# Performance work log

Hardware: AMD Instinct MI355X
Metric: run time of the kernel (lower is better)

Reference implementation:

```python
import jax, jax.numpy as jnp
import numpy as np

EMB = 1024
HEADS = 16
HEAD_SZ = 64
INNER = 4 * EMB
EPS = 1e-5


def layer_norm(x, g, b):
    mu = jnp.mean(x, axis=-1, keepdims=True)
    var = jnp.mean(jnp.square(x - mu), axis=-1, keepdims=True)
    return (x - mu) * jax.lax.rsqrt(var + EPS) * g + b


def setup_inputs() -> dict:
    key = jax.random.key(0)
    ks = jax.random.split(key, 12)
    s = 1.0 / np.sqrt(EMB)
    si = 1.0 / np.sqrt(INNER)
    return {
        "x": jax.random.normal(ks[0], (4, 2048, EMB), dtype=jnp.float32),
        "Wq": jax.random.uniform(ks[1], (EMB, HEADS * HEAD_SZ), jnp.float32, -s, s),
        "Wk": jax.random.uniform(ks[2], (EMB, HEADS * HEAD_SZ), jnp.float32, -s, s),
        "Wv": jax.random.uniform(ks[3], (EMB, HEADS * HEAD_SZ), jnp.float32, -s, s),
        "Wo": jax.random.uniform(ks[4], (HEADS * HEAD_SZ, EMB), jnp.float32, -s, s),
        "bo": jax.random.uniform(ks[5], (EMB,), jnp.float32, -s, s),
        "g1": jnp.ones((EMB,), jnp.float32),
        "b1": jnp.zeros((EMB,), jnp.float32),
        "W1": jax.random.uniform(ks[6], (EMB, INNER), jnp.float32, -s, s),
        "bf1": jax.random.uniform(ks[7], (INNER,), jnp.float32, -s, s),
        "W2": jax.random.uniform(ks[8], (INNER, EMB), jnp.float32, -si, si),
        "bf2": jax.random.uniform(ks[9], (EMB,), jnp.float32, -si, si),
        "g2": jnp.ones((EMB,), jnp.float32),
        "b2": jnp.zeros((EMB,), jnp.float32),
    }


def reference(x, Wq, Wk, Wv, Wo, bo, g1, b1, W1, bf1, W2, bf2, g2, b2):
    bs, seq, _ = x.shape
    # QKV projections -> [b, h, s, d]
    def split_heads(t):
        return t.reshape(bs, seq, HEADS, HEAD_SZ).transpose(0, 2, 1, 3)
    q = split_heads(x @ Wq)
    k = split_heads(x @ Wk)
    v = split_heads(x @ Wv)
    # scaled dot-product attention (vanilla, no mask; pdrop=0)
    attn = jnp.einsum("bhqd,bhkd->bhqk", q, k) / np.sqrt(HEAD_SZ)
    attn = jax.nn.softmax(attn, axis=-1)
    out = jnp.einsum("bhqk,bhkd->bhqd", attn, v)
    out = out.transpose(0, 2, 1, 3).reshape(bs, seq, HEADS * HEAD_SZ)
    out = out @ Wo + bo
    # residual + post-LN
    h = layer_norm(x + out, g1, b1)
    # FFN
    ff = jax.nn.relu(h @ W1 + bf1) @ W2 + bf2
    return layer_norm(h + ff, g2, b2)
```

## Files before the change

kernel.cpp:

```cpp
#include <hip/hip_runtime.h>
#include <stdint.h>

#define DEVI __device__ __forceinline__

typedef __attribute__((ext_vector_type(8))) short bf16x8;
typedef __attribute__((ext_vector_type(4))) float f32x4;
typedef unsigned short u16;
typedef uint32_t u32;

constexpr int EMB = 1024, SEQ = 2048, NTOK = 8192;
constexpr int HEADS = 16, HD = 64, INNER = 4096;

DEVI u16 f2b(float f) {
  u32 u = __float_as_uint(f);
  return (u16)((u + 0x7FFFu + ((u >> 16) & 1u)) >> 16);
}

DEVI u32 pk2(float lo, float hi) {
  u32 r;
  asm("v_cvt_pk_bf16_f32 %0, %1, %2" : "=v"(r) : "v"(lo), "v"(hi));
  return r;
}

DEVI float exp2v(float x) {
  float r;
  asm("v_exp_f32 %0, %1" : "=v"(r) : "v"(x));
  return r;
}

DEVI void gload16(const void* g, void* l) {
  __builtin_amdgcn_global_load_lds(
      (const __attribute__((address_space(1))) void*)g,
      (__attribute__((address_space(3))) void*)l, 16, 0, 0);
}

DEVI int xcd_swz(int bid, int nwg) { return (bid & 7) * (nwg >> 3) + (bid >> 3); }

DEVI int vperm(int k) {
  int g = (k >> 2) & 3, j = k & 3, s2 = k >> 4;
  return ((s2 >> 1) << 5) + (g << 3) + ((s2 & 1) << 2) + j;
}

__global__ __launch_bounds__(256) void k_cvt(const float* __restrict__ src,
                                             u16* __restrict__ dst, int n4) {
  int i = blockIdx.x * 256 + threadIdx.x;
  if (i >= n4) return;
  float4 v = ((const float4*)src)[i];
  ushort4 o = {f2b(v.x), f2b(v.y), f2b(v.z), f2b(v.w)};
  ((ushort4*)dst)[i] = o;
}

__global__ __launch_bounds__(256) void k_cvtT(const float* __restrict__ src,
                                              u16* __restrict__ dst, int K, int N) {
  __shared__ float t[32][33];
  int bk = blockIdx.x % (K >> 5), bn = blockIdx.x / (K >> 5);
  int tx = threadIdx.x & 31, ty = threadIdx.x >> 5;
#pragma unroll
  for (int i = 0; i < 4; i++)
    t[ty + i * 8][tx] = src[(size_t)(bk * 32 + ty + i * 8) * N + bn * 32 + tx];
  __syncthreads();
#pragma unroll
  for (int i = 0; i < 4; i++)
    dst[(size_t)(bn * 32 + ty + i * 8) * K + bk * 32 + tx] = f2b(t[tx][ty + i * 8]);
}

template <int EPI>
__global__ __launch_bounds__(512, 2) void k_gemm8(
    const u16* __restrict__ A, const u16* __restrict__ BT, int M, int N, int K,
    u16* __restrict__ ob0, u16* __restrict__ ob1, u16* __restrict__ ob2,
    float* __restrict__ of0, const float* __restrict__ bias,
    const float* __restrict__ res) {
  __shared__ u16 LDS[3][24576];
  const int tid = threadIdx.x;
  const int lane = tid & 63, w = tid >> 6;
  const int wr = w >> 1, wc = w & 1;
  const int g = lane >> 4, c = lane & 15;
  const int nbx = N >> 7;
  const int bid = xcd_swz(blockIdx.x, gridDim.x);
  const int by = bid / nbx, bx = bid % nbx;
  const int row0 = by << 8, col0 = bx << 7;
  const int NK = K >> 6;

  const f32x4 z4 = {0.f, 0.f, 0.f, 0.f};
  f32x4 acc[4][4];
#pragma unroll
  for (int m = 0; m < 4; m++)
#pragma unroll
    for (int n = 0; n < 4; n++) acc[m][n] = z4;

  auto stageA = [&](int t) {
    const int k0 = t << 6;
    char* base = (char*)&LDS[t % 3][0];
#pragma unroll
    for (int i = 0; i < 4; i++) {
      int s = tid + (i << 9);
      int r = s >> 3, cb = s & 7;
      gload16(A + (size_t)(row0 + r) * K + (k0 + ((cb ^ (r & 7)) << 3)),
              base + s * 16);
    }
  };
  auto stageB = [&](int t) {
    const int k0 = t << 6;
    char* base = (char*)&LDS[t % 3][0] + 32768;
#pragma unroll
    for (int i = 0; i < 2; i++) {
      int s = tid + (i << 9);
      int r = s >> 3, cb = s & 7;
      gload16(BT + (size_t)(col0 + r) * K + (k0 + ((cb ^ (r & 7)) << 3)),
              base + s * 16);
    }
  };

  stageA(0); stageB(0);
  stageA(1); stageB(1);
  asm volatile("s_waitcnt vmcnt(6)" ::: "memory");
  __builtin_amdgcn_s_barrier();

  for (int t = 0; t < NK; t++) {
    const char* Ab = (const char*)&LDS[t % 3][0];
    const char* Bb = Ab + 32768;

    bf16x8 af[4][2], bfr[2][2];
#pragma unroll
    for (int m = 0; m < 4; m++)
#pragma unroll
      for (int kk = 0; kk < 2; kk++) {
        int r = wr * 64 + m * 16 + c;
        af[m][kk] = *(const bf16x8*)(Ab + ((r * 128 + kk * 64 + g * 16) ^ ((r & 7) << 4)));
      }
#pragma unroll
    for (int ni = 0; ni < 2; ni++)
#pragma unroll
      for (int kk = 0; kk < 2; kk++) {
        int rb = wc * 64 + ni * 16 + c;
        bfr[ni][kk] = *(const bf16x8*)(Bb + ((rb * 128 + kk * 64 + g * 16) ^ ((rb & 7) << 4)));
      }
    if (t + 2 < NK) stageA(t + 2);
    __builtin_amdgcn_sched_barrier(0);
    __builtin_amdgcn_s_barrier();
    asm volatile("s_waitcnt lgkmcnt(0)" ::: "memory");
    __builtin_amdgcn_sched_barrier(0);
    __builtin_amdgcn_s_setprio(1);
#pragma unroll
    for (int m = 0; m < 4; m++)
#pragma unroll
      for (int ni = 0; ni < 2; ni++)
#pragma unroll
        for (int kk = 0; kk < 2; kk++)
          acc[m][ni] = __builtin_amdgcn_mfma_f32_16x16x32_bf16(af[m][kk], bfr[ni][kk],
                                                               acc[m][ni], 0, 0, 0);
    __builtin_amdgcn_s_setprio(0);
    __builtin_amdgcn_sched_barrier(0);
    __builtin_amdgcn_s_barrier();

#pragma unroll
    for (int ni = 0; ni < 2; ni++)
#pragma unroll
      for (int kk = 0; kk < 2; kk++) {
        int rb = wc * 64 + 32 + ni * 16 + c;
        bfr[ni][kk] = *(const bf16x8*)(Bb + ((rb * 128 + kk * 64 + g * 16) ^ ((rb & 7) << 4)));
      }
    if (t + 2 < NK) stageB(t + 2);
    __builtin_amdgcn_sched_barrier(0);
    __builtin_amdgcn_s_barrier();
    asm volatile("s_waitcnt lgkmcnt(0)" ::: "memory");
    __builtin_amdgcn_sched_barrier(0);
    __builtin_amdgcn_s_setprio(1);
#pragma unroll
    for (int m = 0; m < 4; m++)
#pragma unroll
      for (int ni = 0; ni < 2; ni++)
#pragma unroll
        for (int kk = 0; kk < 2; kk++)
          acc[m][2 + ni] = __builtin_amdgcn_mfma_f32_16x16x32_bf16(af[m][kk], bfr[ni][kk],
                                                                   acc[m][2 + ni], 0, 0, 0);
    __builtin_amdgcn_s_setprio(0);
    __builtin_amdgcn_sched_barrier(0);
    if (t + 2 < NK)
      asm volatile("s_waitcnt vmcnt(6)" ::: "memory");
    else if (t + 1 < NK)
      asm volatile("s_waitcnt vmcnt(0)" ::: "memory");
    __builtin_amdgcn_s_barrier();
  }

#pragma unroll
  for (int m = 0; m < 4; m++) {
#pragma unroll
    for (int n = 0; n < 4; n++) {
      int ocol = col0 + wc * 64 + n * 16 + c;
      int orow_base = row0 + wr * 64 + m * 16 + 4 * g;
      if constexpr (EPI == 0) {
        int which = ocol >> 10, rem = ocol & 1023;
        int h = rem >> 6, d = rem & 63;
        if (which == 2) {
          int b = orow_base >> 11, sl = orow_base & 2047;
          int blk = sl & ~63, k4 = sl & 63;
          int p = vperm(k4);
          int bh = b * HEADS + h;
          ushort4 vv = {f2b(acc[m][n][0]), f2b(acc[m][n][1]),
                        f2b(acc[m][n][2]), f2b(acc[m][n][3])};
          *(ushort4*)(ob2 + ((size_t)bh * HD + d) * SEQ + blk + p) = vv;
        } else {
#pragma unroll
          for (int r = 0; r < 4; r++) {
            int orow = orow_base + r;
            int b = orow >> 11, s = orow & 2047;
            int bh = b * HEADS + h;
            float av = acc[m][n][r];
            if (which == 0)
              ob0[((size_t)bh * SEQ + s) * HD + d] = f2b(av * 0.1803368801111244f);
            else
              ob1[((size_t)bh * SEQ + s) * HD + d] = f2b(av);
          }
        }
      } else if constexpr (EPI == 1) {
        float bia = bias[ocol];
#pragma unroll
        for (int r = 0; r < 4; r++) {
          int orow = orow_base + r;
          of0[(size_t)orow * N + ocol] =
              acc[m][n][r] + bia + res[(size_t)orow * N + ocol];
        }
      } else if constexpr (EPI == 2) {
        float bia = bias[ocol];
#pragma unroll
        for (int r = 0; r < 4; r++) {
          int orow = orow_base + r;
          float v = acc[m][n][r] + bia;
          ob0[(size_t)orow * N + ocol] = f2b(v > 0.f ? v : 0.f);
        }
      } else {
        float bia = bias[ocol];
#pragma unroll
        for (int r = 0; r < 4; r++) {
          int orow = orow_base + r;
          of0[(size_t)orow * N + ocol] = acc[m][n][r] + bia;
        }
      }
    }
  }
}

__global__ __launch_bounds__(256, 4) void k_attn(const u16* __restrict__ q,
                                                 const u16* __restrict__ kb,
                                                 const u16* __restrict__ vT,
                                                 u16* __restrict__ attn) {
  __shared__ u16 Ks[2][64 * 64];
  __shared__ u16 Vs[2][64 * 64];
  const int tid = threadIdx.x, lane = tid & 63, w = tid >> 6;
  const int g = lane >> 4, c = lane & 15;
  const int blk = xcd_swz(blockIdx.x, gridDim.x);
  const int bh = blk >> 5, qb = blk & 31;
  const int b = bh >> 4, h = bh & 15;
  const u16* qh = q + (size_t)bh * SEQ * HD;
  const u16* kh = kb + (size_t)bh * SEQ * HD;
  const u16* vh = vT + (size_t)bh * HD * SEQ;
  const int qr = qb * 64 + w * 16 + c;
  bf16x8 qf0 = *(const bf16x8*)(qh + (size_t)qr * HD + 8 * g);
  bf16x8 qf1 = *(const bf16x8*)(qh + (size_t)qr * HD + 32 + 8 * g);

  const f32x4 z4 = {0.f, 0.f, 0.f, 0.f};
  f32x4 O[4];
#pragma unroll
  for (int m = 0; m < 4; m++) O[m] = z4;
  float mI = -3.0e38f, lI = 0.f;

  auto stage = [&](int kt, int buf) {
    const int kv0 = kt * 64;
#pragma unroll
    for (int i = 0; i < 2; i++) {
      int s = tid + (i << 8);
      int r = s >> 3, cb = s & 7;
      gload16(kh + (size_t)(kv0 + r) * HD + ((cb ^ (r & 7)) << 3),
              (char*)Ks[buf] + s * 16);
    }
#pragma unroll
    for (int i = 0; i < 2; i++) {
      int s = tid + (i << 8);
      int r = s >> 3, cb = s & 7;
      gload16(vh + (size_t)r * SEQ + kv0 + ((cb ^ (r & 7)) << 3),
              (char*)Vs[buf] + s * 16);
    }
  };

  stage(0, 0);
  __syncthreads();
  int cur = 0;
  constexpr int NT = SEQ / 64;
  for (int kt = 0; kt < NT; kt++) {
    if (kt + 1 < NT) stage(kt + 1, cur ^ 1);

    const char* ksb = (const char*)Ks[cur];
    f32x4 sc[4];
    __builtin_amdgcn_s_setprio(1);
#pragma unroll
    for (int m = 0; m < 4; m++) {
      int r = 16 * m + c;
      int sw = (r & 7) << 4;
      bf16x8 kf0 = *(const bf16x8*)(ksb + ((r * 128 + g * 16) ^ sw));
      bf16x8 kf1 = *(const bf16x8*)(ksb + ((r * 128 + 64 + g * 16) ^ sw));
      f32x4 a = z4;
      a = __builtin_amdgcn_mfma_f32_16x16x32_bf16(kf0, qf0, a, 0, 0, 0);
      a = __builtin_amdgcn_mfma_f32_16x16x32_bf16(kf1, qf1, a, 0, 0, 0);
      sc[m] = a;
    }
    __builtin_amdgcn_s_setprio(0);

    float mx = sc[0][0];
#pragma unroll
    for (int m = 0; m < 4; m++)
#pragma unroll
      for (int r = 0; r < 4; r++) mx = fmaxf(mx, sc[m][r]);
    mx = fmaxf(mx, __shfl_xor(mx, 16));
    mx = fmaxf(mx, __shfl_xor(mx, 32));
    if (!__all(mx - mI <= 8.f)) {
      float mNew = fmaxf(mI, mx);
      float alpha = exp2v(mI - mNew);
      lI *= alpha;
#pragma unroll
      for (int m = 0; m < 4; m++)
#pragma unroll
        for (int r = 0; r < 4; r++) O[m][r] *= alpha;
      mI = mNew;
    }
    float p[4][4];
    float rs = 0.f;
#pragma unroll
    for (int m = 0; m < 4; m++)
#pragma unroll
      for (int r = 0; r < 4; r++) {
        p[m][r] = exp2v(sc[m][r] - mI);
        rs += p[m][r];
      }
    rs += __shfl_xor(rs, 16);
    rs += __shfl_xor(rs, 32);
    lI += rs;

    union V8w { bf16x8 v; u32 w4[4]; };
    V8w pa0, pa1;
    pa0.w4[0] = pk2(p[0][0], p[0][1]); pa0.w4[1] = pk2(p[0][2], p[0][3]);
    pa0.w4[2] = pk2(p[1][0], p[1][1]); pa0.w4[3] = pk2(p[1][2], p[1][3]);
    pa1.w4[0] = pk2(p[2][0], p[2][1]); pa1.w4[1] = pk2(p[2][2], p[2][3]);
    pa1.w4[2] = pk2(p[3][0], p[3][1]); pa1.w4[3] = pk2(p[3][2], p[3][3]);

    const char* vsb = (const char*)Vs[cur];
    __builtin_amdgcn_s_setprio(1);
#pragma unroll
    for (int m = 0; m < 4; m++) {
      int d = 16 * m + c;
      int sw = (d & 7) << 4;
      bf16x8 v0 = *(const bf16x8*)(vsb + ((d * 128 + g * 16) ^ sw));
      bf16x8 v1 = *(const bf16x8*)(vsb + ((d * 128 + 64 + g * 16) ^ sw));
      O[m] = __builtin_amdgcn_mfma_f32_16x16x32_bf16(v0, pa0.v, O[m], 0, 0, 0);
      O[m] = __builtin_amdgcn_mfma_f32_16x16x32_bf16(v1, pa1.v, O[m], 0, 0, 0);
    }
    __builtin_amdgcn_s_setprio(0);

    __syncthreads();
    cur ^= 1;
  }

  float inv = 1.f / lI;
#pragma unroll
  for (int m = 0; m < 4; m++) {
    ushort4 ov = {f2b(O[m][0] * inv), f2b(O[m][1] * inv),
                  f2b(O[m][2] * inv), f2b(O[m][3] * inv)};
    int col = h * 64 + 16 * m + 4 * g;
    *(ushort4*)(attn + ((size_t)(b * SEQ + qr)) * EMB + col) = ov;
  }
}

__global__ __launch_bounds__(256) void k_ln1(const float* __restrict__ y,
                                             const float* __restrict__ gw,
                                             const float* __restrict__ bw,
                                             float* __restrict__ hf,
                                             u16* __restrict__ hb) {
  const int row = blockIdx.x, tid = threadIdx.x, lane = tid & 63, w = tid >> 6;
  const float4 v = ((const float4*)(y + (size_t)row * EMB))[tid];
  float s = v.x + v.y + v.z + v.w;
  float s2 = v.x * v.x + v.y * v.y + v.z * v.z + v.w * v.w;
#pragma unroll
  for (int m = 1; m < 64; m <<= 1) {
    s += __shfl_xor(s, m);
    s2 += __shfl_xor(s2, m);
  }
  __shared__ float rs_[4], rq_[4];
  if (lane == 0) { rs_[w] = s; rq_[w] = s2; }
  __syncthreads();
  s = rs_[0] + rs_[1] + rs_[2] + rs_[3];
  s2 = rq_[0] + rq_[1] + rq_[2] + rq_[3];
  const float mu = s * (1.f / EMB);
  const float var = s2 * (1.f / EMB) - mu * mu;
  const float rstd = rsqrtf(var + 1e-5f);
  const float4 gg = ((const float4*)gw)[tid];
  const float4 bb = ((const float4*)bw)[tid];
  float4 o;
  o.x = (v.x - mu) * rstd * gg.x + bb.x;
  o.y = (v.y - mu) * rstd * gg.y + bb.y;
  o.z = (v.z - mu) * rstd * gg.z + bb.z;
  o.w = (v.w - mu) * rstd * gg.w + bb.w;
  ((float4*)(hf + (size_t)row * EMB))[tid] = o;
  ushort4 ob = {f2b(o.x), f2b(o.y), f2b(o.z), f2b(o.w)};
  ((ushort4*)(hb + (size_t)row * EMB))[tid] = ob;
}

__global__ __launch_bounds__(256) void k_ln2(const float* __restrict__ hf,
                                             const float* __restrict__ z,
                                             const float* __restrict__ gw,
                                             const float* __restrict__ bw,
                                             float* __restrict__ outp) {
  const int row = blockIdx.x, tid = threadIdx.x, lane = tid & 63, w = tid >> 6;
  float4 v = ((const float4*)(hf + (size_t)row * EMB))[tid];
  const float4 zz = ((const float4*)(z + (size_t)row * EMB))[tid];
  v.x += zz.x; v.y += zz.y; v.z += zz.z; v.w += zz.w;
  float s = v.x + v.y + v.z + v.w;
  float s2 = v.x * v.x + v.y * v.y + v.z * v.z + v.w * v.w;
#pragma unroll
  for (int m = 1; m < 64; m <<= 1) {
    s += __shfl_xor(s, m);
    s2 += __shfl_xor(s2, m);
  }
  __shared__ float rs_[4], rq_[4];
  if (lane == 0) { rs_[w] = s; rq_[w] = s2; }
  __syncthreads();
  s = rs_[0] + rs_[1] + rs_[2] + rs_[3];
  s2 = rq_[0] + rq_[1] + rq_[2] + rq_[3];
  const float mu = s * (1.f / EMB);
  const float var = s2 * (1.f / EMB) - mu * mu;
  const float rstd = rsqrtf(var + 1e-5f);
  const float4 gg = ((const float4*)gw)[tid];
  const float4 bb = ((const float4*)bw)[tid];
  float4 o;
  o.x = (v.x - mu) * rstd * gg.x + bb.x;
  o.y = (v.y - mu) * rstd * gg.y + bb.y;
  o.z = (v.z - mu) * rstd * gg.z + bb.z;
  o.w = (v.w - mu) * rstd * gg.w + bb.w;
  ((float4*)(outp + (size_t)row * EMB))[tid] = o;
}

extern "C" void kernel_launch(void* const* d_in, const int* in_sizes, int n_in,
                              void* d_out, int out_size, void* d_ws, size_t ws_size,
                              hipStream_t stream) {
  const float* x = (const float*)d_in[0];
  const float* Wq = (const float*)d_in[1];
  const float* Wk = (const float*)d_in[2];
  const float* Wv = (const float*)d_in[3];
  const float* Wo = (const float*)d_in[4];
  const float* bo = (const float*)d_in[5];
  const float* g1 = (const float*)d_in[6];
  const float* b1 = (const float*)d_in[7];
  const float* W1 = (const float*)d_in[8];
  const float* bf1 = (const float*)d_in[9];
  const float* W2 = (const float*)d_in[10];
  const float* bf2 = (const float*)d_in[11];
  const float* g2 = (const float*)d_in[12];
  const float* b2 = (const float*)d_in[13];
  float* out = (float*)d_out;

  char* ws = (char*)d_ws;
  size_t off = 0;
  auto alloc = [&](size_t bytes) {
    char* p = ws + off;
    off += (bytes + 255) & ~(size_t)255;
    return p;
  };
  u16* xb = (u16*)alloc((size_t)NTOK * EMB * 2);
  u16* wqkvT = (u16*)alloc((size_t)3072 * 1024 * 2);
  u16* qB = (u16*)alloc((size_t)NTOK * EMB * 2);
  u16* kB = (u16*)alloc((size_t)NTOK * EMB * 2);
  u16* vTB = (u16*)alloc((size_t)NTOK * EMB * 2);
  u16* woT = (u16*)alloc((size_t)1024 * 1024 * 2);
  u16* w1T = (u16*)alloc((size_t)4096 * 1024 * 2);
  u16* w2T = (u16*)alloc((size_t)1024 * 4096 * 2);
  float* y = (float*)alloc((size_t)NTOK * EMB * 4);
  u16* ff1 = (u16*)alloc((size_t)NTOK * INNER * 2);
  u16* attn = xb;
  float* hf = (float*)qB;
  u16* hb = vTB;
  float* z = y;

  k_cvt<<<NTOK * EMB / 4 / 256, 256, 0, stream>>>(x, xb, NTOK * EMB / 4);
  k_cvtT<<<1024, 256, 0, stream>>>(Wq, wqkvT, 1024, 1024);
  k_cvtT<<<1024, 256, 0, stream>>>(Wk, wqkvT + 1048576, 1024, 1024);
  k_cvtT<<<1024, 256, 0, stream>>>(Wv, wqkvT + 2097152, 1024, 1024);
  k_cvtT<<<1024, 256, 0, stream>>>(Wo, woT, 1024, 1024);
  k_cvtT<<<4096, 256, 0, stream>>>(W1, w1T, 1024, 4096);
  k_cvtT<<<4096, 256, 0, stream>>>(W2, w2T, 4096, 1024);
  k_gemm8<0><<<(NTOK / 256) * (3072 / 128), 512, 0, stream>>>(
      xb, wqkvT, NTOK, 3072, 1024, qB, kB, vTB, nullptr, nullptr, nullptr);
  k_attn<<<64 * 32, 256, 0, stream>>>(qB, kB, vTB, attn);
  k_gemm8<1><<<(NTOK / 256) * (1024 / 128), 512, 0, stream>>>(
      attn, woT, NTOK, 1024, 1024, nullptr, nullptr, nullptr, y, bo, x);
  k_ln1<<<NTOK, 256, 0, stream>>>(y, g1, b1, hf, hb);
  k_gemm8<2><<<(NTOK / 256) * (4096 / 128), 512, 0, stream>>>(
      hb, w1T, NTOK, 4096, 1024, ff1, nullptr, nullptr, nullptr, bf1, nullptr);
  k_gemm8<3><<<(NTOK / 256) * (1024 / 128), 512, 0, stream>>>(
      ff1, w2T, NTOK, 1024, 4096, nullptr, nullptr, nullptr, z, bf2, nullptr);
  k_ln2<<<NTOK, 256, 0, stream>>>(hf, z, g2, b2, out);
}
```

Before: 538.6 us.

## Add 256x256-tile GEMM kernel for QKV and FFN1 projections

```diff
diff --git a/kernel.cpp b/kernel.cpp
--- a/kernel.cpp
+++ b/kernel.cpp
@@ -62,6 +62,217 @@
 #pragma unroll
   for (int i = 0; i < 4; i++)
     dst[(size_t)(bn * 32 + ty + i * 8) * K + bk * 32 + tx] = f2b(t[tx][ty + i * 8]);
+}
+
+template <int EPI>
+__global__ __launch_bounds__(512, 2) void k_g256(
+    const u16* __restrict__ A, const u16* __restrict__ BT, int M, int N, int K,
+    u16* __restrict__ ob0, u16* __restrict__ ob1, u16* __restrict__ ob2,
+    float* __restrict__ of0, const float* __restrict__ bias,
+    const float* __restrict__ res) {
+  __shared__ u16 LDS[81920];
+  const int tid = threadIdx.x;
+  const int lane = tid & 63, w = tid >> 6;
+  const int wr = w >> 2, wc = w & 3;
+  const int g = lane >> 4, c = lane & 15;
+  const int nbx = N >> 8;
+  const int bid = xcd_swz(blockIdx.x, gridDim.x);
+  const int by = bid / nbx, bx = bid % nbx;
+  const int row0 = by << 8, col0 = bx << 8;
+  const int NK = K >> 6;
+
+  const f32x4 z4 = {0.f, 0.f, 0.f, 0.f};
+  f32x4 acc[8][4];
+#pragma unroll
+  for (int m = 0; m < 8; m++)
+#pragma unroll
+    for (int n = 0; n < 4; n++) acc[m][n] = z4;
+
+  auto stA = [&](int t, int h) {
+    const int k0 = t << 6;
+    char* base = (char*)LDS + (t % 3) * 32768 + h * 16384;
+#pragma unroll
+    for (int i = 0; i < 2; i++) {
+      int s = tid + (i << 9);
+      int r = (h << 7) + (s >> 3), cb = s & 7;
+      gload16(A + (size_t)(row0 + r) * K + (k0 + ((cb ^ (r & 7)) << 3)),
+              base + s * 16);
+    }
+  };
+  auto stB = [&](int t, int h) {
+    const int k0 = t << 6;
+    char* base = (char*)LDS + 98304 + (t & 1) * 32768 + h * 16384;
+#pragma unroll
+    for (int i = 0; i < 2; i++) {
+      int s = tid + (i << 9);
+      int r = (h << 7) + (s >> 3), cb = s & 7;
+      gload16(BT + (size_t)(col0 + r) * K + (k0 + ((cb ^ (r & 7)) << 3)),
+              base + s * 16);
+    }
+  };
+  auto rdA = [&](const char* Ab, int row, int kk) {
+    return *(const bf16x8*)(Ab + ((row * 128 + kk * 64 + g * 16) ^ ((row & 7) << 4)));
+  };
+
+  stA(0, 0); stA(0, 1);
+  stB(0, 0); stB(0, 1);
+  stA(1, 0); stA(1, 1);
+  asm volatile("s_waitcnt vmcnt(4)" ::: "memory");
+  __builtin_amdgcn_s_barrier();
+  __builtin_amdgcn_sched_barrier(0);
+
+  for (int t = 0; t < NK; t++) {
+    const char* Ab = (const char*)LDS + (t % 3) * 32768;
+    const char* Bb = (const char*)LDS + 98304 + (t & 1) * 32768;
+    bf16x8 af[4][2], b0[2][2], b1[2][2];
+
+#pragma unroll
+    for (int m = 0; m < 4; m++)
+#pragma unroll
+      for (int kk = 0; kk < 2; kk++) af[m][kk] = rdA(Ab, wr * 128 + m * 16 + c, kk);
+#pragma unroll
+    for (int n = 0; n < 2; n++)
+#pragma unroll
+      for (int kk = 0; kk < 2; kk++) b0[n][kk] = rdA(Bb, wc * 64 + n * 16 + c, kk);
+    if (t + 1 < NK) stB(t + 1, 0);
+    asm volatile("s_waitcnt lgkmcnt(8)" ::: "memory");
+    __builtin_amdgcn_sched_barrier(0);
+    __builtin_amdgcn_s_barrier();
+    asm volatile("s_waitcnt lgkmcnt(0)" ::: "memory");
+    __builtin_amdgcn_sched_barrier(0);
+    __builtin_amdgcn_s_setprio(1);
+#pragma unroll
+    for (int m = 0; m < 4; m++)
+#pragma unroll
+      for (int n = 0; n < 2; n++)
+#pragma unroll
+        for (int kk = 0; kk < 2; kk++)
+          acc[m][n] = __builtin_amdgcn_mfma_f32_16x16x32_bf16(af[m][kk], b0[n][kk],
+                                                              acc[m][n], 0, 0, 0);
+    __builtin_amdgcn_s_setprio(0);
+    __builtin_amdgcn_sched_barrier(0);
+    __builtin_amdgcn_s_barrier();
+
+#pragma unroll
+    for (int n = 0; n < 2; n++)
+#pragma unroll
+      for (int kk = 0; kk < 2; kk++)
+        b1[n][kk] = rdA(Bb, wc * 64 + 32 + n * 16 + c, kk);
+    if (t + 1 < NK) stB(t + 1, 1);
+    __builtin_amdgcn_sched_barrier(0);
+    __builtin_amdgcn_s_barrier();
+    asm volatile("s_waitcnt lgkmcnt(0)" ::: "memory");
+    __builtin_amdgcn_sched_barrier(0);
+    __builtin_amdgcn_s_setprio(1);
+#pragma unroll
+    for (int m = 0; m < 4; m++)
+#pragma unroll
+      for (int n = 0; n < 2; n++)
+#pragma unroll
+        for (int kk = 0; kk < 2; kk++)
+          acc[m][2 + n] = __builtin_amdgcn_mfma_f32_16x16x32_bf16(af[m][kk], b1[n][kk],
+                                                                  acc[m][2 + n], 0, 0, 0);
+    __builtin_amdgcn_s_setprio(0);
+    __builtin_amdgcn_sched_barrier(0);
+    __builtin_amdgcn_s_barrier();
+
+#pragma unroll
+    for (int m = 0; m < 4; m++)
+#pragma unroll
+      for (int kk = 0; kk < 2; kk++)
+        af[m][kk] = rdA(Ab, wr * 128 + 64 + m * 16 + c, kk);
+    if (t + 2 < NK) stA(t + 2, 0);
+    __builtin_amdgcn_sched_barrier(0);
+    __builtin_amdgcn_s_barrier();
+    asm volatile("s_waitcnt lgkmcnt(0)" ::: "memory");
+    __builtin_amdgcn_sched_barrier(0);
+    __builtin_amdgcn_s_setprio(1);
+#pragma unroll
+    for (int m = 0; m < 4; m++)
+#pragma unroll
+      for (int n = 0; n < 2; n++)
+#pragma unroll
+        for (int kk = 0; kk < 2; kk++)
+          acc[4 + m][n] = __builtin_amdgcn_mfma_f32_16x16x32_bf16(af[m][kk], b0[n][kk],
+                                                                  acc[4 + m][n], 0, 0, 0);
+    __builtin_amdgcn_s_setprio(0);
+    __builtin_amdgcn_sched_barrier(0);
+    __builtin_amdgcn_s_barrier();
+
+    if (t + 2 < NK) stA(t + 2, 1);
+    __builtin_amdgcn_sched_barrier(0);
+    __builtin_amdgcn_s_barrier();
+    __builtin_amdgcn_s_setprio(1);
+#pragma unroll
+    for (int m = 0; m < 4; m++)
+#pragma unroll
+      for (int n = 0; n < 2; n++)
+#pragma unroll
+        for (int kk = 0; kk < 2; kk++)
+          acc[4 + m][2 + n] = __builtin_amdgcn_mfma_f32_16x16x32_bf16(
+              af[m][kk], b1[n][kk], acc[4 + m][2 + n], 0, 0, 0);
+    __builtin_amdgcn_s_setprio(0);
+    __builtin_amdgcn_sched_barrier(0);
+    if (t + 2 < NK)
+      asm volatile("s_waitcnt vmcnt(4)" ::: "memory");
+    else if (t + 1 < NK)
+      asm volatile("s_waitcnt vmcnt(0)" ::: "memory");
+    __builtin_amdgcn_s_barrier();
+    __builtin_amdgcn_sched_barrier(0);
+  }
+
+#pragma unroll
+  for (int m = 0; m < 8; m++) {
+#pragma unroll
+    for (int n = 0; n < 4; n++) {
+      int ocol = col0 + wc * 64 + n * 16 + c;
+      int orow_base = row0 + wr * 128 + m * 16 + 4 * g;
+      if constexpr (EPI == 0) {
+        int which = ocol >> 10, rem = ocol & 1023;
+        int h = rem >> 6, d = rem & 63;
+        if (which == 2) {
+          int b = orow_base >> 11, sl = orow_base & 2047;
+          int blk = sl & ~63, k4 = sl & 63;
+          int p = vperm(k4);
+          int bh = b * HEADS + h;
+          ushort4 vv = {f2b(acc[m][n][0]), f2b(acc[m][n][1]),
+                        f2b(acc[m][n][2]), f2b(acc[m][n][3])};
+          *(ushort4*)(ob2 + ((size_t)bh * HD + d) * SEQ + blk + p) = vv;
+        } else {
+#pragma unroll
+          for (int r = 0; r < 4; r++) {
+            int orow = orow_base + r;
+            int b = orow >> 11, s = orow & 2047;
+            int bh = b * HEADS + h;
+            float av = acc[m][n][r];
+            if (which == 0)
+              ob0[((size_t)bh * SEQ + s) * HD + d] = f2b(av * 0.1803368801111244f);
+            else
+              ob1[((size_t)bh * SEQ + s) * HD + d] = f2b(av);
+          }
+        }
+      } else if constexpr (EPI == 2) {
+        float bia = bias[ocol];
+#pragma unroll
+        for (int r = 0; r < 4; r++) {
+          int orow = orow_base + r;
+          float v = acc[m][n][r] + bia;
+          ob0[(size_t)orow * N + ocol] = f2b(v > 0.f ? v : 0.f);
+        }
+      } else {
+        float bia = bias[ocol];
+#pragma unroll
+        for (int r = 0; r < 4; r++) {
+          int orow = orow_base + r;
+          float v = acc[m][n][r] + bia;
+          if constexpr (EPI == 1)
+            of0[(size_t)orow * N + ocol] = v + res[(size_t)orow * N + ocol];
+          else
+            of0[(size_t)orow * N + ocol] = v;
+        }
+      }
+    }
+  }
 }
 
 template <int EPI>
@@ -189,45 +400,13 @@
     for (int n = 0; n < 4; n++) {
       int ocol = col0 + wc * 64 + n * 16 + c;
       int orow_base = row0 + wr * 64 + m * 16 + 4 * g;
-      if constexpr (EPI == 0) {
-        int which = ocol >> 10, rem = ocol & 1023;
-        int h = rem >> 6, d = rem & 63;
-        if (which == 2) {
-          int b = orow_base >> 11, sl = orow_base & 2047;
-          int blk = sl & ~63, k4 = sl & 63;
-          int p = vperm(k4);
-          int bh = b * HEADS + h;
-          ushort4 vv = {f2b(acc[m][n][0]), f2b(acc[m][n][1]),
-                        f2b(acc[m][n][2]), f2b(acc[m][n][3])};
-          *(ushort4*)(ob2 + ((size_t)bh * HD + d) * SEQ + blk + p) = vv;
-        } else {
-#pragma unroll
-          for (int r = 0; r < 4; r++) {
-            int orow = orow_base + r;
-            int b = orow >> 11, s = orow & 2047;
-            int bh = b * HEADS + h;
-            float av = acc[m][n][r];
-            if (which == 0)
-              ob0[((size_t)bh * SEQ + s) * HD + d] = f2b(av * 0.1803368801111244f);
-            else
-              ob1[((size_t)bh * SEQ + s) * HD + d] = f2b(av);
-          }
-        }
-      } else if constexpr (EPI == 1) {
+      if constexpr (EPI == 1) {
         float bia = bias[ocol];
 #pragma unroll
         for (int r = 0; r < 4; r++) {
           int orow = orow_base + r;
           of0[(size_t)orow * N + ocol] =
               acc[m][n][r] + bia + res[(size_t)orow * N + ocol];
-        }
-      } else if constexpr (EPI == 2) {
-        float bia = bias[ocol];
-#pragma unroll
-        for (int r = 0; r < 4; r++) {
-          int orow = orow_base + r;
-          float v = acc[m][n][r] + bia;
-          ob0[(size_t)orow * N + ocol] = f2b(v > 0.f ? v : 0.f);
         }
       } else {
         float bia = bias[ocol];
@@ -486,13 +665,13 @@
   k_cvtT<<<1024, 256, 0, stream>>>(Wo, woT, 1024, 1024);
   k_cvtT<<<4096, 256, 0, stream>>>(W1, w1T, 1024, 4096);
   k_cvtT<<<4096, 256, 0, stream>>>(W2, w2T, 4096, 1024);
-  k_gemm8<0><<<(NTOK / 256) * (3072 / 128), 512, 0, stream>>>(
+  k_g256<0><<<(NTOK / 256) * (3072 / 256), 512, 0, stream>>>(
       xb, wqkvT, NTOK, 3072, 1024, qB, kB, vTB, nullptr, nullptr, nullptr);
   k_attn<<<64 * 32, 256, 0, stream>>>(qB, kB, vTB, attn);
   k_gemm8<1><<<(NTOK / 256) * (1024 / 128), 512, 0, stream>>>(
       attn, woT, NTOK, 1024, 1024, nullptr, nullptr, nullptr, y, bo, x);
   k_ln1<<<NTOK, 256, 0, stream>>>(y, g1, b1, hf, hb);
-  k_gemm8<2><<<(NTOK / 256) * (4096 / 128), 512, 0, stream>>>(
+  k_g256<2><<<(NTOK / 256) * (4096 / 256), 512, 0, stream>>>(
       hb, w1T, NTOK, 4096, 1024, ff1, nullptr, nullptr, nullptr, bf1, nullptr);
   k_gemm8<3><<<(NTOK / 256) * (1024 / 128), 512, 0, stream>>>(
       ff1, w2T, NTOK, 1024, 4096, nullptr, nullptr, nullptr, z, bf2, nullptr);
```

Result: no change. 534.7 us (-0.7%).
